# Kernel tuning notes

Hardware: AMD Instinct MI355X
Metric: run time of the kernel (lower is better)

Reference implementation:

```python
import jax, jax.numpy as jnp
import numpy as np

TEMPERATURE = 8.0  # sqrt(d_k=64)
NEG = -1e15


def setup_inputs() -> dict:
    key = jax.random.key(0)
    k1, k2, k3, k4, k5 = jax.random.split(key, 5)
    BH, L, D = 64, 1024, 64  # B=4 examples x H=16 heads
    B = 4
    q = jax.random.normal(k1, (BH, L, D), dtype=jnp.float32)
    k = jax.random.normal(k2, (BH, L, D), dtype=jnp.float32)
    v = jax.random.normal(k3, (BH, L, D), dtype=jnp.float32)
    mask = jax.random.randint(k4, (BH, L, L), 0, 2).astype(jnp.bool_)
    edge = jax.random.randint(k5, (B, L, L), 0, 2).astype(jnp.int32)
    return {"q": q, "k": k, "v": v, "mask": mask, "edge": edge}


def reference(q, k, v, mask, edge):
    # attn = q @ k^T / temperature : [BH, L, L]
    attn = jnp.einsum('bld,bmd->blm', q, k) / TEMPERATURE
    # edge.repeat(BH // B, 1, 1): torch repeat == tile along batch dim
    rep = attn.shape[0] // edge.shape[0]
    edge_t = jnp.tile(edge, (rep, 1, 1))
    attn = jnp.where(edge_t == 0, NEG, attn)
    attn = jnp.where(mask, NEG, attn)
    attn = jax.nn.softmax(attn, axis=2)
    # dropout p=0 -> identity
    output = jnp.einsum('blm,bmd->bld', attn, v)
    return (output, attn)
```

## Files before the change

kernel.cpp:

```cpp
#include <hip/hip_runtime.h>
#include <hip/hip_bf16.h>

#define L_ 1024
#define BH_ 64
#define NEGV (-1e15f)
#define QSCALE 0.18033688011112043f

typedef float f32x4 __attribute__((ext_vector_type(4)));
typedef short s16x8 __attribute__((ext_vector_type(8)));
typedef unsigned short ushort_t;

__device__ __forceinline__ unsigned short f2bf(float f) {
    return __builtin_bit_cast(unsigned short, __float2bfloat16(f));
}
__device__ __forceinline__ unsigned selw(uint4 v, int i) {
    switch (i) { case 0: return v.x; case 1: return v.y; case 2: return v.z; default: return v.w; }
}
__device__ __forceinline__ unsigned spread4(unsigned n) {
    return (n & 1u) | ((n & 2u) << 3) | ((n & 4u) << 6) | ((n & 8u) << 9);
}
__device__ __forceinline__ unsigned pack_bytes_nz(uint4 m) {
    unsigned u = 0;
    #pragma unroll
    for (int k = 0; k < 4; ++k) {
        const unsigned x = selw(m, k);
        u |= ((x & 0x000000FFu) ? 1u : 0u) << (k * 4 + 0);
        u |= ((x & 0x0000FF00u) ? 1u : 0u) << (k * 4 + 1);
        u |= ((x & 0x00FF0000u) ? 1u : 0u) << (k * 4 + 2);
        u |= ((x & 0xFF000000u) ? 1u : 0u) << (k * 4 + 3);
    }
    return u;
}

template<bool TESTZERO>
__device__ __forceinline__ unsigned row_bits_i32(uint4 e0, uint4 e1, uint4 e2, uint4 e3, int ln)
{
    #define BAL_(v) (TESTZERO ? __ballot((v) == 0u) : __ballot((v) != 0u))
    const unsigned long long b00 = BAL_(e0.x), b01 = BAL_(e0.y), b02 = BAL_(e0.z), b03 = BAL_(e0.w);
    const unsigned long long b10 = BAL_(e1.x), b11 = BAL_(e1.y), b12 = BAL_(e1.z), b13 = BAL_(e1.w);
    const unsigned long long b20 = BAL_(e2.x), b21 = BAL_(e2.y), b22 = BAL_(e2.z), b23 = BAL_(e2.w);
    const unsigned long long b30 = BAL_(e3.x), b31 = BAL_(e3.y), b32 = BAL_(e3.z), b33 = BAL_(e3.w);
    #undef BAL_
    const int q0 = ln >> 4, sh = (ln & 15) << 2;
    unsigned u = 0;
    unsigned long long bp;
    bp = q0 == 0 ? b00 : q0 == 1 ? b10 : q0 == 2 ? b20 : b30;
    u |= spread4((unsigned)((bp >> sh) & 0xF)) << 0;
    bp = q0 == 0 ? b01 : q0 == 1 ? b11 : q0 == 2 ? b21 : b31;
    u |= spread4((unsigned)((bp >> sh) & 0xF)) << 1;
    bp = q0 == 0 ? b02 : q0 == 1 ? b12 : q0 == 2 ? b22 : b32;
    u |= spread4((unsigned)((bp >> sh) & 0xF)) << 2;
    bp = q0 == 0 ? b03 : q0 == 1 ? b13 : q0 == 2 ? b23 : b33;
    u |= spread4((unsigned)((bp >> sh) & 0xF)) << 3;
    return u;
}

__global__ __launch_bounds__(256)
void prep(const float* __restrict__ qp, const float* __restrict__ kp,
          const float* __restrict__ vp, const unsigned char* __restrict__ maskp,
          const int* __restrict__ edgep, ushort_t* __restrict__ ws)
{
    __shared__ float tile[128][68];
    ushort_t* Kp = ws;
    ushort_t* Vp = ws + (1u << 22);
    ushort_t* Qp = ws + (2u << 22);
    ushort_t* Mp = ws + (3u << 22);

    const int b = blockIdx.x;
    const int t = threadIdx.x;

    if (b < 512) {
        const int bh = b >> 3, kt = b & 7;
        const int r = t >> 1, h = t & 1;
        const float* src = kp + (((size_t)((bh << 10) + (kt << 7) + r)) << 6) + (h << 5);
        float v[32];
        #pragma unroll
        for (int j = 0; j < 8; ++j) *(float4*)&v[j << 2] = *((const float4*)src + j);
        ushort_t* dst = Kp + ((size_t)((bh << 3) + kt) << 13) + (r << 6);
        #pragma unroll
        for (int q = 0; q < 4; ++q) {
            const int c = (h << 2) + q;
            const int s = c ^ (r & 7);
            s16x8 o;
            #pragma unroll
            for (int j = 0; j < 8; ++j) o[j] = (short)f2bf(v[(q << 3) + j]);
            *(s16x8*)(dst + (s << 3)) = o;
        }
    } else if (b < 1024) {
        const int idx = b - 512;
        const int bh = idx >> 3, vt = idx & 7;
        const float* vsrc = vp + (((size_t)(bh << 10) + (vt << 7)) << 6);
        #pragma unroll
        for (int i = 0; i < 8; ++i) {
            const int f4 = (i << 8) + t;
            const int k = f4 >> 4, d4 = f4 & 15;
            *(float4*)&tile[k][d4 << 2] = *((const float4*)vsrc + f4);
        }
        __syncthreads();
        ushort_t* dst = Vp + ((size_t)((bh << 3) + vt) << 13);
        #pragma unroll
        for (int i = 0; i < 4; ++i) {
            const int ci = (t << 2) + i;
            const int d = ci >> 4, p = ci & 15;
            const int c = p ^ (d & 7);
            s16x8 o;
            #pragma unroll
            for (int j = 0; j < 8; ++j) o[j] = (short)f2bf(tile[(c << 3) + j][d]);
            *(s16x8*)(dst + (ci << 3)) = o;
        }
    } else if (b < 1088) {
        const int bh = b - 1024;
        const int wv = t >> 6, ln = t & 63;
        for (int i = 0; i < 16; ++i) {
            const int rt = (i << 2) + wv;
            const int r = (rt << 4) + (ln & 15), gq = ln >> 4;
            const float* src = qp + (((size_t)((bh << 10) + r)) << 6) + (gq << 3);
            const float4 q0 = *(const float4*)src;
            const float4 q1 = *(const float4*)(src + 4);
            const float4 q2 = *(const float4*)(src + 32);
            const float4 q3 = *(const float4*)(src + 36);
            s16x8 a, bfr;
            a[0]=(short)f2bf(q0.x*QSCALE); a[1]=(short)f2bf(q0.y*QSCALE);
            a[2]=(short)f2bf(q0.z*QSCALE); a[3]=(short)f2bf(q0.w*QSCALE);
            a[4]=(short)f2bf(q1.x*QSCALE); a[5]=(short)f2bf(q1.y*QSCALE);
            a[6]=(short)f2bf(q1.z*QSCALE); a[7]=(short)f2bf(q1.w*QSCALE);
            bfr[0]=(short)f2bf(q2.x*QSCALE); bfr[1]=(short)f2bf(q2.y*QSCALE);
            bfr[2]=(short)f2bf(q2.z*QSCALE); bfr[3]=(short)f2bf(q2.w*QSCALE);
            bfr[4]=(short)f2bf(q3.x*QSCALE); bfr[5]=(short)f2bf(q3.y*QSCALE);
            bfr[6]=(short)f2bf(q3.z*QSCALE); bfr[7]=(short)f2bf(q3.w*QSCALE);
            ushort_t* dst = Qp + ((size_t)((bh << 6) + rt) << 10) + (ln << 4);
            *(s16x8*)(dst) = a;
            *(s16x8*)(dst + 8) = bfr;
        }
    } else {
        const int wv = t >> 6, ln = t & 63;
        const int rid = b - 1088;
        const int eb = rid >> 10, row = rid & 1023;

        unsigned det = 0;
        const unsigned* mu = (const unsigned*)maskp;
        #pragma unroll
        for (int i = 0; i < 16; ++i) det |= mu[i];
        const bool mask_i32 = ((det & 0xFFFFFF00u) == 0u);

        unsigned ewv;
        {
            const int rb = ((eb << 10) + row) << 10;
            const uint4 e0 = *((const uint4*)(edgep + rb) + ln);
            const uint4 e1 = *((const uint4*)(edgep + rb + 256) + ln);
            const uint4 e2 = *((const uint4*)(edgep + rb + 512) + ln);
            const uint4 e3 = *((const uint4*)(edgep + rb + 768) + ln);
            ewv = row_bits_i32<true>(e0, e1, e2, e3, ln);
        }
        const int pp = ((ln & 7) << 3) + (ln >> 3);
        #pragma unroll
        for (int i = 0; i < 4; ++i) {
            const int bq = (wv << 2) + i;
            const int bh = (bq << 2) + eb;
            unsigned u = ewv;
            if (!mask_i32) {
                const uint4 m = *((const uint4*)(maskp + ((size_t)((bh << 10) + row) << 10)) + ln);
                u |= pack_bytes_nz(m);
            } else {
                const int* mp = (const int*)maskp + ((size_t)((bh << 10) + row) << 10);
                const uint4 m0 = *((const uint4*)mp + ln);
                const uint4 m1 = *((const uint4*)(mp + 256) + ln);
                const uint4 m2 = *((const uint4*)(mp + 512) + ln);
                const uint4 m3 = *((const uint4*)(mp + 768) + ln);
                u |= row_bits_i32<false>(m0, m1, m2, m3, ln);
            }
            Mp[((size_t)((bh << 10) + row) << 6) + pp] = (ushort_t)u;
        }
    }
}

__global__ __launch_bounds__(512, 5)
void attn_main(const ushort_t* __restrict__ ws, float* __restrict__ outO,
               float* __restrict__ outA)
{
    __shared__ __align__(16) ushort_t p_lds[16 * 1024];
    __shared__ float part[16][8];
    __shared__ float gred[16];
    __shared__ float opart[4][16][17];

    const ushort_t* Kp = ws;
    const ushort_t* Vp = ws + (1u << 22);
    const ushort_t* Qp = ws + (2u << 22);
    const ushort_t* Mp = ws + (3u << 22);

    const int tid = threadIdx.x, lane = tid & 63, w = tid >> 6;
    const int g = lane >> 4, ln = lane & 15;
    const int bid = blockIdx.x, xcd = bid & 7, slot = bid >> 3;
    const int bh = xcd + ((slot >> 6) << 3);
    const int rt = slot & 63;
    const int r0 = rt << 4;
    const int rw = (w << 4) + ln;
    const int ksw = rw & 7, vsw = ln & 7;
    const int dt = w & 3, kh = w >> 2;

    const ushort_t* qs = Qp + ((size_t)((bh << 6) + rt) << 10) + (lane << 4);
    const s16x8 a0 = *(const s16x8*)(qs);
    const s16x8 a1 = *(const s16x8*)(qs + 8);

    uint4 br[4];
    #pragma unroll
    for (int reg = 0; reg < 4; ++reg)
        br[reg] = *(const uint4*)(Mp + ((size_t)((bh << 10) + r0 + (g << 2) + reg) << 6) + (w << 3));

    const ushort_t* kbase = Kp + ((size_t)bh << 16) + (rw << 6);
    const int ko0 = (g ^ ksw) << 3, ko1 = ((4 + g) ^ ksw) << 3;
    const ushort_t* vrow = Vp + ((size_t)bh << 16) + (((dt << 4) + ln) << 7);
    const int vo0 = (((kh << 3) + g) ^ vsw) << 3, vo1 = (((kh << 3) + 4 + g) ^ vsw) << 3;

    #define LK(tt, oo) (*(const s16x8*)(kbase + ((tt) << 13) + (oo)))
    #define LV(tt, oo) (*(const s16x8*)(vrow  + ((tt) << 13) + (oo)))

    s16x8 kc0 = LK(0, ko0), kc1 = LK(0, ko1);
    s16x8 kn0 = LK(1, ko0), kn1 = LK(1, ko1);
    s16x8 va0, va1, vn0, vn1;

    float rs[4] = {0.f, 0.f, 0.f, 0.f};

    #pragma unroll
    for (int kt = 0; kt < 8; ++kt) {
        const s16x8 b0 = kc0, b1 = kc1;
        kc0 = kn0; kc1 = kn1;
        if (kt < 6) {
            kn0 = LK(kt + 2, ko0); kn1 = LK(kt + 2, ko1);
        } else if (kt == 6) {
            va0 = LV(0, vo0); va1 = LV(0, vo1);
        } else {
            vn0 = LV(1, vo0); vn1 = LV(1, vo1);
        }

        f32x4 acc = {0.f, 0.f, 0.f, 0.f};
        acc = __builtin_amdgcn_mfma_f32_16x16x32_bf16(a0, b0, acc, 0, 0, 0);
        acc = __builtin_amdgcn_mfma_f32_16x16x32_bf16(a1, b1, acc, 0, 0, 0);

        #pragma unroll
        for (int reg = 0; reg < 4; ++reg) {
            const unsigned ew = selw(br[reg], kt >> 1);
            float sv = acc[reg];
            if ((ew >> (((kt & 1) << 4) + ln)) & 1u) sv = NEGV;
            const float e = __builtin_amdgcn_exp2f(sv);
            rs[reg] += e;
            const int prow = (g << 2) + reg;
            char* pd = (char*)p_lds + (prow << 11)
                     + ((((kt << 4) + (w << 1) + (ln >> 3)) ^ (prow & 7)) << 4)
                     + ((ln & 7) << 1);
            *(ushort_t*)pd = f2bf(e);
        }
    }

    #pragma unroll
    for (int reg = 0; reg < 4; ++reg) {
        float s = rs[reg];
        s += __shfl_xor(s, 1);
        s += __shfl_xor(s, 2);
        s += __shfl_xor(s, 4);
        s += __shfl_xor(s, 8);
        if (ln == 0) part[(g << 2) + reg][w] = s;
    }
    __syncthreads();
    if (tid < 16) {
        float s = part[tid][0];
        #pragma unroll
        for (int i = 1; i < 8; ++i) s += part[tid][i];
        gred[tid] = __builtin_amdgcn_rcpf(s);
    }
    __syncthreads();

    f32x4 acco = {0.f, 0.f, 0.f, 0.f};
    #pragma unroll
    for (int ut = 0; ut < 8; ++ut) {
        const s16x8 b0 = va0, b1 = va1;
        va0 = vn0; va1 = vn1;
        if (ut < 6) {
            vn0 = LV(ut + 2, vo0); vn1 = LV(ut + 2, vo1);
        }
        const char* pl = (const char*)p_lds + (ln << 11);
        const s16x8 pa0 = *(const s16x8*)(pl + ((((ut << 4) + (kh << 3) + g)     ^ vsw) << 4));
        const s16x8 pa1 = *(const s16x8*)(pl + ((((ut << 4) + (kh << 3) + 4 + g) ^ vsw) << 4));
        acco = __builtin_amdgcn_mfma_f32_16x16x32_bf16(pa0, b0, acco, 0, 0, 0);
        acco = __builtin_amdgcn_mfma_f32_16x16x32_bf16(pa1, b1, acco, 0, 0, 0);
    }
    #undef LK
    #undef LV

    if (kh == 1) {
        #pragma unroll
        for (int reg = 0; reg < 4; ++reg)
            opart[dt][(g << 2) + reg][ln] = acco[reg];
    }
    __syncthreads();
    if (kh == 0) {
        #pragma unroll
        for (int reg = 0; reg < 4; ++reg) {
            const int rl = (g << 2) + reg;
            outO[((size_t)((bh << 10) + r0 + rl) << 6) + (dt << 4) + ln] =
                (acco[reg] + opart[dt][rl][ln]) * gred[rl];
        }
    }

    {
        const char* src = (const char*)p_lds;
        float* dstf = outA + ((size_t)((bh << 10) + r0) << 10);
        #pragma unroll
        for (int i = 0; i < 4; ++i) {
            const unsigned boff = (unsigned)((i * 512 + tid) << 4);
            const int rl = (int)(boff >> 11);
            const float rinv = gred[rl];
            const uint4 d4 = *(const uint4*)(src + (boff ^ ((rl & 7) << 4)));
            float4 f0, f1;
            f0.x = __builtin_bit_cast(float, d4.x << 16) * rinv;
            f0.y = __builtin_bit_cast(float, d4.x & 0xFFFF0000u) * rinv;
            f0.z = __builtin_bit_cast(float, d4.y << 16) * rinv;
            f0.w = __builtin_bit_cast(float, d4.y & 0xFFFF0000u) * rinv;
            f1.x = __builtin_bit_cast(float, d4.z << 16) * rinv;
            f1.y = __builtin_bit_cast(float, d4.z & 0xFFFF0000u) * rinv;
            f1.z = __builtin_bit_cast(float, d4.w << 16) * rinv;
            f1.w = __builtin_bit_cast(float, d4.w & 0xFFFF0000u) * rinv;
            char* db = (char*)dstf + ((size_t)boff << 1);
            *(float4*)db = f0;
            *(float4*)(db + 16) = f1;
        }
    }
}

__global__ __launch_bounds__(512)
void attn_fb(const float* __restrict__ qp, const float* __restrict__ kp,
             const float* __restrict__ vp, const unsigned char* __restrict__ maskp,
             const int* __restrict__ edgep, float* __restrict__ outO,
             float* __restrict__ outA)
{
    __shared__ __align__(16) ushort_t p_lds[16 * 1024];
    __shared__ float part[16][8];
    __shared__ float gred[16];
    __shared__ float opart[4][16][17];

    const int tid = threadIdx.x, lane = tid & 63, w = tid >> 6;
    const int g = lane >> 4, ln = lane & 15;
    const int bid = blockIdx.x, xcd = bid & 7, slot = bid >> 3;
    const int bh = xcd + ((slot >> 6) << 3);
    const int r0 = (slot & 63) << 4;
    const int c0 = w << 7;

    unsigned det = 0;
    const unsigned* mu = (const unsigned*)maskp;
    #pragma unroll
    for (int i = 0; i < 16; ++i) det |= mu[i];
    const bool mask_i32 = ((det & 0xFFFFFF00u) == 0u);

    const float* qb = qp + (((size_t)((bh << 10) + r0 + ln)) << 6) + (g << 3);
    s16x8 a0, a1;
    #pragma unroll
    for (int j = 0; j < 8; ++j) {
        a0[j] = (short)f2bf(qb[j] * QSCALE);
        a1[j] = (short)f2bf(qb[j + 32] * QSCALE);
    }

    f32x4 acc[8];
    #pragma unroll
    for (int nt = 0; nt < 8; ++nt) acc[nt] = (f32x4){0.f, 0.f, 0.f, 0.f};
    #pragma unroll
    for (int nt = 0; nt < 8; ++nt) {
        const float* kb = kp + (((size_t)((bh << 10) + c0 + (nt << 4) + ln)) << 6) + (g << 3);
        s16x8 b0, b1;
        #pragma unroll
        for (int j = 0; j < 8; ++j) {
            b0[j] = (short)f2bf(kb[j]);
            b1[j] = (short)f2bf(kb[j + 32]);
        }
        acc[nt] = __builtin_amdgcn_mfma_f32_16x16x32_bf16(a0, b0, acc[nt], 0, 0, 0);
        acc[nt] = __builtin_amdgcn_mfma_f32_16x16x32_bf16(a1, b1, acc[nt], 0, 0, 0);
    }

    float rs[4] = {0.f, 0.f, 0.f, 0.f};
    #pragma unroll
    for (int reg = 0; reg < 4; ++reg) {
        const int row = r0 + (g << 2) + reg;
        #pragma unroll
        for (int nt = 0; nt < 8; ++nt) {
            const int col = c0 + (nt << 4) + ln;
            float sv = acc[nt][reg];
            int mv;
            if (mask_i32) mv = ((const int*)maskp)[((size_t)((bh << 10) + row) << 10) + col];
            else          mv = (int)maskp[((size_t)((bh << 10) + row) << 10) + col];
            if (edgep[((size_t)((((bh & 3) << 10) + row)) << 10) + col] == 0 || mv != 0) sv = NEGV;
            const float e = __builtin_amdgcn_exp2f(sv);
            rs[reg] += e;
            const int rl = (g << 2) + reg;
            const unsigned off = ((unsigned)((rl << 11) | (col << 1))) ^ ((rl & 7) << 4);
            *(ushort_t*)((char*)p_lds + off) = f2bf(e);
        }
    }
    #pragma unroll
    for (int reg = 0; reg < 4; ++reg) {
        float s = rs[reg];
        s += __shfl_xor(s, 1);
        s += __shfl_xor(s, 2);
        s += __shfl_xor(s, 4);
        s += __shfl_xor(s, 8);
        if (ln == 0) part[(g << 2) + reg][w] = s;
    }
    __syncthreads();
    if (tid < 16) {
        float s = part[tid][0];
        #pragma unroll
        for (int i = 1; i < 8; ++i) s += part[tid][i];
        gred[tid] = __builtin_amdgcn_rcpf(s);
    }
    __syncthreads();

    const int dt = w & 3, kh = w >> 2;
    f32x4 acco = {0.f, 0.f, 0.f, 0.f};
    for (int kt = 0; kt < 16; ++kt) {
        const int ktg = (kh << 4) + kt;
        const unsigned offA = ((unsigned)((ln << 11) | (ktg << 6) | (g << 4))) ^ ((ln & 7) << 4);
        const s16x8 pa = *(const s16x8*)((const char*)p_lds + offA);
        s16x8 vb;
        #pragma unroll
        for (int j = 0; j < 8; ++j)
            vb[j] = (short)f2bf(vp[((size_t)((bh << 10) + (ktg << 5) + (g << 3) + j) << 6) + (dt << 4) + ln]);
        acco = __builtin_amdgcn_mfma_f32_16x16x32_bf16(pa, vb, acco, 0, 0, 0);
    }
    if (kh == 1) {
        #pragma unroll
        for (int reg = 0; reg < 4; ++reg)
            opart[dt][(g << 2) + reg][ln] = acco[reg];
    }
    __syncthreads();
    if (kh == 0) {
        #pragma unroll
        for (int reg = 0; reg < 4; ++reg) {
            const int rl = (g << 2) + reg;
            outO[((size_t)((bh << 10) + r0 + rl) << 6) + (dt << 4) + ln] =
                (acco[reg] + opart[dt][rl][ln]) * gred[rl];
        }
    }
    {
        const char* src = (const char*)p_lds;
        float* dstf = outA + ((size_t)((bh << 10) + r0) << 10);
        #pragma unroll
        for (int i = 0; i < 4; ++i) {
            const unsigned boff = (unsigned)((i * 512 + tid) << 4);
            const int rl = (int)(boff >> 11);
            const float rinv = gred[rl];
            const uint4 d4 = *(const uint4*)(src + (boff ^ ((rl & 7) << 4)));
            float4 f0, f1;
            f0.x = __builtin_bit_cast(float, d4.x << 16) * rinv;
            f0.y = __builtin_bit_cast(float, d4.x & 0xFFFF0000u) * rinv;
            f0.z = __builtin_bit_cast(float, d4.y << 16) * rinv;
            f0.w = __builtin_bit_cast(float, d4.y & 0xFFFF0000u) * rinv;
            f1.x = __builtin_bit_cast(float, d4.z << 16) * rinv;
            f1.y = __builtin_bit_cast(float, d4.z & 0xFFFF0000u) * rinv;
            f1.z = __builtin_bit_cast(float, d4.w << 16) * rinv;
            f1.w = __builtin_bit_cast(float, d4.w & 0xFFFF0000u) * rinv;
            char* db = (char*)dstf + ((size_t)boff << 1);
            *(float4*)db = f0;
            *(float4*)(db + 16) = f1;
        }
    }
}

extern "C" void kernel_launch(void* const* d_in, const int* in_sizes, int n_in,
                              void* d_out, int out_size, void* d_ws, size_t ws_size,
                              hipStream_t stream)
{
    (void)in_sizes; (void)n_in; (void)out_size;
    const float* qp = (const float*)d_in[0];
    const float* kp = (const float*)d_in[1];
    const float* vp = (const float*)d_in[2];
    const unsigned char* maskp = (const unsigned char*)d_in[3];
    const int* edgep = (const int*)d_in[4];

    float* outO = (float*)d_out;
    float* outA = outO + ((long long)BH_ * L_ * 64);

    const size_t need = (size_t)32 * 1024 * 1024;
    if (d_ws != nullptr && ws_size >= need) {
        ushort_t* ws = (ushort_t*)d_ws;
        prep<<<5184, 256, 0, stream>>>(qp, kp, vp, maskp, edgep, ws);
        attn_main<<<4096, 512, 0, stream>>>(ws, outO, outA);
    } else {
        attn_fb<<<4096, 512, 0, stream>>>(qp, kp, vp, maskp, edgep, outO, outA);
    }
}
```

Measured before the change: 216.6 us.

## Specialize warps: four compute PV, four write attention matrix concurrently

The PV matmul in attn_main now runs only on waves 0-3, each handling a full 16-column slice of D over all 1024 keys. Waves 4-7 meanwhile convert the bf16 probabilities in LDS to fp32 and stream the attention matrix to global memory. This removes the cross-wave partial-sum reduction through shared memory and its barrier, and overlaps the large attention store with the PV compute. In exchange, per-wave MFMA work doubles on half the waves and the store work doubles on the other half, so balance depends on which part dominates.

```diff
diff --git a/kernel.cpp b/kernel.cpp
--- a/kernel.cpp
+++ b/kernel.cpp
@@ -181,7 +181,6 @@
     __shared__ __align__(16) ushort_t p_lds[16 * 1024];
     __shared__ float part[16][8];
     __shared__ float gred[16];
-    __shared__ float opart[4][16][17];
 
     const ushort_t* Kp = ws;
     const ushort_t* Vp = ws + (1u << 22);
@@ -196,7 +195,6 @@
     const int r0 = rt << 4;
     const int rw = (w << 4) + ln;
     const int ksw = rw & 7, vsw = ln & 7;
-    const int dt = w & 3, kh = w >> 2;
 
     const ushort_t* qs = Qp + ((size_t)((bh << 6) + rt) << 10) + (lane << 4);
     const s16x8 a0 = *(const s16x8*)(qs);
@@ -209,15 +207,17 @@
 
     const ushort_t* kbase = Kp + ((size_t)bh << 16) + (rw << 6);
     const int ko0 = (g ^ ksw) << 3, ko1 = ((4 + g) ^ ksw) << 3;
-    const ushort_t* vrow = Vp + ((size_t)bh << 16) + (((dt << 4) + ln) << 7);
-    const int vo0 = (((kh << 3) + g) ^ vsw) << 3, vo1 = (((kh << 3) + 4 + g) ^ vsw) << 3;
+    const int dt2 = w & 3;
+    const ushort_t* vrow = Vp + ((size_t)bh << 16) + (((dt2 << 4) + ln) << 7);
+    const int voA0 = ((0 + g) ^ vsw) << 3,  voA1 = ((4 + g) ^ vsw) << 3;
+    const int voB0 = ((8 + g) ^ vsw) << 3,  voB1 = ((12 + g) ^ vsw) << 3;
 
     #define LK(tt, oo) (*(const s16x8*)(kbase + ((tt) << 13) + (oo)))
     #define LV(tt, oo) (*(const s16x8*)(vrow  + ((tt) << 13) + (oo)))
 
     s16x8 kc0 = LK(0, ko0), kc1 = LK(0, ko1);
     s16x8 kn0 = LK(1, ko0), kn1 = LK(1, ko1);
-    s16x8 va0, va1, vn0, vn1;
+    s16x8 vc0, vc1, vn0, vn1;
 
     float rs[4] = {0.f, 0.f, 0.f, 0.f};
 
@@ -228,9 +228,9 @@
         if (kt < 6) {
             kn0 = LK(kt + 2, ko0); kn1 = LK(kt + 2, ko1);
         } else if (kt == 6) {
-            va0 = LV(0, vo0); va1 = LV(0, vo1);
+            if (w < 4) { vc0 = LV(0, voA0); vc1 = LV(0, voA1); }
         } else {
-            vn0 = LV(1, vo0); vn1 = LV(1, vo1);
+            if (w < 4) { vn0 = LV(0, voB0); vn1 = LV(0, voB1); }
         }
 
         f32x4 acc = {0.f, 0.f, 0.f, 0.f};
@@ -270,23 +270,156 @@
     }
     __syncthreads();
 
-    f32x4 acco = {0.f, 0.f, 0.f, 0.f};
-    #pragma unroll
-    for (int ut = 0; ut < 8; ++ut) {
-        const s16x8 b0 = va0, b1 = va1;
-        va0 = vn0; va1 = vn1;
-        if (ut < 6) {
-            vn0 = LV(ut + 2, vo0); vn1 = LV(ut + 2, vo1);
-        }
-        const char* pl = (const char*)p_lds + (ln << 11);
-        const s16x8 pa0 = *(const s16x8*)(pl + ((((ut << 4) + (kh << 3) + g)     ^ vsw) << 4));
-        const s16x8 pa1 = *(const s16x8*)(pl + ((((ut << 4) + (kh << 3) + 4 + g) ^ vsw) << 4));
-        acco = __builtin_amdgcn_mfma_f32_16x16x32_bf16(pa0, b0, acco, 0, 0, 0);
-        acco = __builtin_amdgcn_mfma_f32_16x16x32_bf16(pa1, b1, acco, 0, 0, 0);
+    if (w < 4) {
+        f32x4 acco = {0.f, 0.f, 0.f, 0.f};
+        #pragma unroll
+        for (int s = 0; s < 16; ++s) {
+            const s16x8 b0 = vc0, b1 = vc1;
+            vc0 = vn0; vc1 = vn1;
+            if (s < 14) {
+                const int s2 = s + 2;
+                const int tl = s2 >> 1;
+                if (s2 & 1) { vn0 = LV(tl, voB0); vn1 = LV(tl, voB1); }
+                else        { vn0 = LV(tl, voA0); vn1 = LV(tl, voA1); }
+            }
+            const int tl = s >> 1, k2 = s & 1;
+            const char* pl = (const char*)p_lds + (ln << 11);
+            const s16x8 pa0 = *(const s16x8*)(pl + ((((tl << 4) + (k2 << 3) + g)     ^ vsw) << 4));
+            const s16x8 pa1 = *(const s16x8*)(pl + ((((tl << 4) + (k2 << 3) + 4 + g) ^ vsw) << 4));
+            acco = __builtin_amdgcn_mfma_f32_16x16x32_bf16(pa0, b0, acco, 0, 0, 0);
+            acco = __builtin_amdgcn_mfma_f32_16x16x32_bf16(pa1, b1, acco, 0, 0, 0);
+        }
+        #pragma unroll
+        for (int reg = 0; reg < 4; ++reg) {
+            const int rl = (g << 2) + reg;
+            outO[((size_t)((bh << 10) + r0 + rl) << 6) + (dt2 << 4) + ln] =
+                acco[reg] * gred[rl];
+        }
+    } else {
+        const int t2 = tid - 256;
+        const char* src = (const char*)p_lds;
+        float* dstf = outA + ((size_t)((bh << 10) + r0) << 10);
+        #pragma unroll
+        for (int i = 0; i < 8; ++i) {
+            const unsigned boff = (unsigned)((i * 256 + t2) << 4);
+            const int rl = (int)(boff >> 11);
+            const float rinv = gred[rl];
+            const uint4 d4 = *(const uint4*)(src + (boff ^ ((rl & 7) << 4)));
+            float4 f0, f1;
+            f0.x = __builtin_bit_cast(float, d4.x << 16) * rinv;
+            f0.y = __builtin_bit_cast(float, d4.x & 0xFFFF0000u) * rinv;
+            f0.z = __builtin_bit_cast(float, d4.y << 16) * rinv;
+            f0.w = __builtin_bit_cast(float, d4.y & 0xFFFF0000u) * rinv;
+            f1.x = __builtin_bit_cast(float, d4.z << 16) * rinv;
+            f1.y = __builtin_bit_cast(float, d4.z & 0xFFFF0000u) * rinv;
+            f1.z = __builtin_bit_cast(float, d4.w << 16) * rinv;
+            f1.w = __builtin_bit_cast(float, d4.w & 0xFFFF0000u) * rinv;
+            char* db = (char*)dstf + ((size_t)boff << 1);
+            *(float4*)db = f0;
+            *(float4*)(db + 16) = f1;
+        }
     }
     #undef LK
     #undef LV
-
+}
+
+__global__ __launch_bounds__(512)
+void attn_fb(const float* __restrict__ qp, const float* __restrict__ kp,
+             const float* __restrict__ vp, const unsigned char* __restrict__ maskp,
+             const int* __restrict__ edgep, float* __restrict__ outO,
+             float* __restrict__ outA)
+{
+    __shared__ __align__(16) ushort_t p_lds[16 * 1024];
+    __shared__ float part[16][8];
+    __shared__ float gred[16];
+    __shared__ float opart[4][16][17];
+
+    const int tid = threadIdx.x, lane = tid & 63, w = tid >> 6;
+    const int g = lane >> 4, ln = lane & 15;
+    const int bid = blockIdx.x, xcd = bid & 7, slot = bid >> 3;
+    const int bh = xcd + ((slot >> 6) << 3);
+    const int r0 = (slot & 63) << 4;
+    const int c0 = w << 7;
+
+    unsigned det = 0;
+    const unsigned* mu = (const unsigned*)maskp;
+    #pragma unroll
+    for (int i = 0; i < 16; ++i) det |= mu[i];
+    const bool mask_i32 = ((det & 0xFFFFFF00u) == 0u);
+
+    const float* qb = qp + (((size_t)((bh << 10) + r0 + ln)) << 6) + (g << 3);
+    s16x8 a0, a1;
+    #pragma unroll
+    for (int j = 0; j < 8; ++j) {
+        a0[j] = (short)f2bf(qb[j] * QSCALE);
+        a1[j] = (short)f2bf(qb[j + 32] * QSCALE);
+    }
+
+    f32x4 acc[8];
+    #pragma unroll
+    for (int nt = 0; nt < 8; ++nt) acc[nt] = (f32x4){0.f, 0.f, 0.f, 0.f};
+    #pragma unroll
+    for (int nt = 0; nt < 8; ++nt) {
+        const float* kb = kp + (((size_t)((bh << 10) + c0 + (nt << 4) + ln)) << 6) + (g << 3);
+        s16x8 b0, b1;
+        #pragma unroll
+        for (int j = 0; j < 8; ++j) {
+            b0[j] = (short)f2bf(kb[j]);
+            b1[j] = (short)f2bf(kb[j + 32]);
+        }
+        acc[nt] = __builtin_amdgcn_mfma_f32_16x16x32_bf16(a0, b0, acc[nt], 0, 0, 0);
+        acc[nt] = __builtin_amdgcn_mfma_f32_16x16x32_bf16(a1, b1, acc[nt], 0, 0, 0);
+    }
+
+    float rs[4] = {0.f, 0.f, 0.f, 0.f};
+    #pragma unroll
+    for (int reg = 0; reg < 4; ++reg) {
+        const int row = r0 + (g << 2) + reg;
+        #pragma unroll
+        for (int nt = 0; nt < 8; ++nt) {
+            const int col = c0 + (nt << 4) + ln;
+            float sv = acc[nt][reg];
+            int mv;
+            if (mask_i32) mv = ((const int*)maskp)[((size_t)((bh << 10) + row) << 10) + col];
+            else          mv = (int)maskp[((size_t)((bh << 10) + row) << 10) + col];
+            if (edgep[((size_t)((((bh & 3) << 10) + row)) << 10) + col] == 0 || mv != 0) sv = NEGV;
+            const float e = __builtin_amdgcn_exp2f(sv);
+            rs[reg] += e;
+            const int rl = (g << 2) + reg;
+            const unsigned off = ((unsigned)((rl << 11) | (col << 1))) ^ ((rl & 7) << 4);
+            *(ushort_t*)((char*)p_lds + off) = f2bf(e);
+        }
+    }
+    #pragma unroll
+    for (int reg = 0; reg < 4; ++reg) {
+        float s = rs[reg];
+        s += __shfl_xor(s, 1);
+        s += __shfl_xor(s, 2);
+        s += __shfl_xor(s, 4);
+        s += __shfl_xor(s, 8);
+        if (ln == 0) part[(g << 2) + reg][w] = s;
+    }
+    __syncthreads();
+    if (tid < 16) {
+        float s = part[tid][0];
+        #pragma unroll
+        for (int i = 1; i < 8; ++i) s += part[tid][i];
+        gred[tid] = __builtin_amdgcn_rcpf(s);
+    }
+    __syncthreads();
+
+    const int dt = w & 3, kh = w >> 2;
+    f32x4 acco = {0.f, 0.f, 0.f, 0.f};
+    for (int kt = 0; kt < 16; ++kt) {
+        const int ktg = (kh << 4) + kt;
+        const unsigned offA = ((unsigned)((ln << 11) | (ktg << 6) | (g << 4))) ^ ((ln & 7) << 4);
+        const s16x8 pa = *(const s16x8*)((const char*)p_lds + offA);
+        s16x8 vb;
+        #pragma unroll
+        for (int j = 0; j < 8; ++j)
+            vb[j] = (short)f2bf(vp[((size_t)((bh << 10) + (ktg << 5) + (g << 3) + j) << 6) + (dt << 4) + ln]);
+        acco = __builtin_amdgcn_mfma_f32_16x16x32_bf16(pa, vb, acco, 0, 0, 0);
+    }
     if (kh == 1) {
         #pragma unroll
         for (int reg = 0; reg < 4; ++reg)
@@ -301,7 +434,6 @@
                 (acco[reg] + opart[dt][rl][ln]) * gred[rl];
         }
     }
-
     {
         const char* src = (const char*)p_lds;
         float* dstf = outA + ((size_t)((bh << 10) + r0) << 10);
@@ -327,142 +459,6 @@
     }
 }
 
-__global__ __launch_bounds__(512)
-void attn_fb(const float* __restrict__ qp, const float* __restrict__ kp,
-             const float* __restrict__ vp, const unsigned char* __restrict__ maskp,
-             const int* __restrict__ edgep, float* __restrict__ outO,
-             float* __restrict__ outA)
-{
-    __shared__ __align__(16) ushort_t p_lds[16 * 1024];
-    __shared__ float part[16][8];
-    __shared__ float gred[16];
-    __shared__ float opart[4][16][17];
-
-    const int tid = threadIdx.x, lane = tid & 63, w = tid >> 6;
-    const int g = lane >> 4, ln = lane & 15;
-    const int bid = blockIdx.x, xcd = bid & 7, slot = bid >> 3;
-    const int bh = xcd + ((slot >> 6) << 3);
-    const int r0 = (slot & 63) << 4;
-    const int c0 = w << 7;
-
-    unsigned det = 0;
-    const unsigned* mu = (const unsigned*)maskp;
-    #pragma unroll
-    for (int i = 0; i < 16; ++i) det |= mu[i];
-    const bool mask_i32 = ((det & 0xFFFFFF00u) == 0u);
-
-    const float* qb = qp + (((size_t)((bh << 10) + r0 + ln)) << 6) + (g << 3);
-    s16x8 a0, a1;
-    #pragma unroll
-    for (int j = 0; j < 8; ++j) {
-        a0[j] = (short)f2bf(qb[j] * QSCALE);
-        a1[j] = (short)f2bf(qb[j + 32] * QSCALE);
-    }
-
-    f32x4 acc[8];
-    #pragma unroll
-    for (int nt = 0; nt < 8; ++nt) acc[nt] = (f32x4){0.f, 0.f, 0.f, 0.f};
-    #pragma unroll
-    for (int nt = 0; nt < 8; ++nt) {
-        const float* kb = kp + (((size_t)((bh << 10) + c0 + (nt << 4) + ln)) << 6) + (g << 3);
-        s16x8 b0, b1;
-        #pragma unroll
-        for (int j = 0; j < 8; ++j) {
-            b0[j] = (short)f2bf(kb[j]);
-            b1[j] = (short)f2bf(kb[j + 32]);
-        }
-        acc[nt] = __builtin_amdgcn_mfma_f32_16x16x32_bf16(a0, b0, acc[nt], 0, 0, 0);
-        acc[nt] = __builtin_amdgcn_mfma_f32_16x16x32_bf16(a1, b1, acc[nt], 0, 0, 0);
-    }
-
-    float rs[4] = {0.f, 0.f, 0.f, 0.f};
-    #pragma unroll
-    for (int reg = 0; reg < 4; ++reg) {
-        const int row = r0 + (g << 2) + reg;
-        #pragma unroll
-        for (int nt = 0; nt < 8; ++nt) {
-            const int col = c0 + (nt << 4) + ln;
-            float sv = acc[nt][reg];
-            int mv;
-            if (mask_i32) mv = ((const int*)maskp)[((size_t)((bh << 10) + row) << 10) + col];
-            else          mv = (int)maskp[((size_t)((bh << 10) + row) << 10) + col];
-            if (edgep[((size_t)((((bh & 3) << 10) + row)) << 10) + col] == 0 || mv != 0) sv = NEGV;
-            const float e = __builtin_amdgcn_exp2f(sv);
-            rs[reg] += e;
-            const int rl = (g << 2) + reg;
-            const unsigned off = ((unsigned)((rl << 11) | (col << 1))) ^ ((rl & 7) << 4);
-            *(ushort_t*)((char*)p_lds + off) = f2bf(e);
-        }
-    }
-    #pragma unroll
-    for (int reg = 0; reg < 4; ++reg) {
-        float s = rs[reg];
-        s += __shfl_xor(s, 1);
-        s += __shfl_xor(s, 2);
-        s += __shfl_xor(s, 4);
-        s += __shfl_xor(s, 8);
-        if (ln == 0) part[(g << 2) + reg][w] = s;
-    }
-    __syncthreads();
-    if (tid < 16) {
-        float s = part[tid][0];
-        #pragma unroll
-        for (int i = 1; i < 8; ++i) s += part[tid][i];
-        gred[tid] = __builtin_amdgcn_rcpf(s);
-    }
-    __syncthreads();
-
-    const int dt = w & 3, kh = w >> 2;
-    f32x4 acco = {0.f, 0.f, 0.f, 0.f};
-    for (int kt = 0; kt < 16; ++kt) {
-        const int ktg = (kh << 4) + kt;
-        const unsigned offA = ((unsigned)((ln << 11) | (ktg << 6) | (g << 4))) ^ ((ln & 7) << 4);
-        const s16x8 pa = *(const s16x8*)((const char*)p_lds + offA);
-        s16x8 vb;
-        #pragma unroll
-        for (int j = 0; j < 8; ++j)
-            vb[j] = (short)f2bf(vp[((size_t)((bh << 10) + (ktg << 5) + (g << 3) + j) << 6) + (dt << 4) + ln]);
-        acco = __builtin_amdgcn_mfma_f32_16x16x32_bf16(pa, vb, acco, 0, 0, 0);
-    }
-    if (kh == 1) {
-        #pragma unroll
-        for (int reg = 0; reg < 4; ++reg)
-            opart[dt][(g << 2) + reg][ln] = acco[reg];
-    }
-    __syncthreads();
-    if (kh == 0) {
-        #pragma unroll
-        for (int reg = 0; reg < 4; ++reg) {
-            const int rl = (g << 2) + reg;
-            outO[((size_t)((bh << 10) + r0 + rl) << 6) + (dt << 4) + ln] =
-                (acco[reg] + opart[dt][rl][ln]) * gred[rl];
-        }
-    }
-    {
-        const char* src = (const char*)p_lds;
-        float* dstf = outA + ((size_t)((bh << 10) + r0) << 10);
-        #pragma unroll
-        for (int i = 0; i < 4; ++i) {
-            const unsigned boff = (unsigned)((i * 512 + tid) << 4);
-            const int rl = (int)(boff >> 11);
-            const float rinv = gred[rl];
-            const uint4 d4 = *(const uint4*)(src + (boff ^ ((rl & 7) << 4)));
-            float4 f0, f1;
-            f0.x = __builtin_bit_cast(float, d4.x << 16) * rinv;
-            f0.y = __builtin_bit_cast(float, d4.x & 0xFFFF0000u) * rinv;
-            f0.z = __builtin_bit_cast(float, d4.y << 16) * rinv;
-            f0.w = __builtin_bit_cast(float, d4.y & 0xFFFF0000u) * rinv;
-            f1.x = __builtin_bit_cast(float, d4.z << 16) * rinv;
-            f1.y = __builtin_bit_cast(float, d4.z & 0xFFFF0000u) * rinv;
-            f1.z = __builtin_bit_cast(float, d4.w << 16) * rinv;
-            f1.w = __builtin_bit_cast(float, d4.w & 0xFFFF0000u) * rinv;
-            char* db = (char*)dstf + ((size_t)boff << 1);
-            *(float4*)db = f0;
-            *(float4*)(db + 16) = f1;
-        }
-    }
-}
-
 extern "C" void kernel_launch(void* const* d_in, const int* in_sizes, int n_in,
                               void* d_out, int out_size, void* d_ws, size_t ws_size,
                               hipStream_t stream)
```

After: 256.3 us. 1.18x slower.
